# Kernel tuning notes

Measured on AMD Instinct MI355X. Metric: run time of the kernel, lower is better.

Reference implementation:

```python
import jax, jax.numpy as jnp
import numpy as np

NUM_EXPERTS = 8
TOP_K = 2

def setup_inputs() -> dict:
    key = jax.random.key(0)
    ks = jax.random.split(key, 5)
    B, S, D, F, E = 4, 2048, 1024, 4096, NUM_EXPERTS
    x = jax.random.normal(ks[0], (B, S, D), dtype=jnp.float32)
    router_w = jax.random.normal(ks[1], (D, E), dtype=jnp.float32) * 0.02
    router_b = jnp.zeros((E,), dtype=jnp.float32)
    w1 = jax.random.normal(ks[2], (E, D, F), dtype=jnp.float32) * 0.02
    b1 = jnp.zeros((E, F), dtype=jnp.float32)
    w2 = jax.random.normal(ks[3], (E, F, D), dtype=jnp.float32) * 0.02
    b2 = jnp.zeros((E, D), dtype=jnp.float32)
    return {"x": x, "router_w": router_w, "router_b": router_b,
            "w1": w1, "b1": b1, "w2": w2, "b2": b2}

def reference(x, router_w, router_b, w1, b1, w2, b2):
    B, S, D = x.shape
    E = router_w.shape[1]
    x_flat = x.reshape(-1, D)                                  # [N, D]
    router_probs = jax.nn.softmax(x_flat @ router_w + router_b, axis=-1)  # [N, E]
    topk_probs, topk_idx = jax.lax.top_k(router_probs, TOP_K)  # [N, K]
    topk_probs = topk_probs / jnp.sum(topk_probs, axis=-1, keepdims=True)
    # combine weight per (token, expert): sum over top-k slots assigned to that expert
    cw = jnp.sum(topk_probs[..., None] * jax.nn.one_hot(topk_idx, E, dtype=x.dtype), axis=1)  # [N, E]
    out = jnp.zeros_like(x_flat)
    for e in range(E):  # small fixed expert count; each iter is a dense GEMM pair
        h = jax.nn.gelu(x_flat @ w1[e] + b1[e], approximate=False)  # [N, F]
        out = out + cw[:, e:e + 1] * (h @ w2[e] + b2[e])            # [N, D]
    return out.reshape(B, S, D)
```

## Files before the change

kernel.cpp:

```cpp
#include <hip/hip_runtime.h>
#include <hip/hip_bf16.h>

typedef __attribute__((ext_vector_type(8))) __bf16 bf16x8;
typedef __attribute__((ext_vector_type(4))) float f32x4;

#define NTOK 8192
#define D_DIM 1024
#define F_DIM 4096
#define NEXP 8
#define SLOT_TOT 16384
#define SLOT_CAP 16640
#define TILE_MAX 136

__device__ __forceinline__ unsigned short f2b(float f) {
  __hip_bfloat16 b = __float2bfloat16(f);
  return reinterpret_cast<unsigned short&>(b);
}

__device__ __forceinline__ float gelu_f(float v) {
  const float y2 = v * (1.5957691216f + 0.0713548162f * v * v);
  return v * __builtin_amdgcn_rcpf(1.f + __expf(-y2));
}

__device__ __forceinline__ void gload_lds16(const void* g, void* l) {
  __builtin_amdgcn_global_load_lds(
      (__attribute__((address_space(1))) void*)g,
      (__attribute__((address_space(3))) void*)l, 16, 0, 0);
}


__global__ void init_counts_kernel(int* counts) {
  if (threadIdx.x < NEXP) counts[threadIdx.x] = 0;
}

__global__ void zero_out_kernel(float* out) {
  const int i = blockIdx.x * 256 + threadIdx.x;
  reinterpret_cast<float4*>(out)[i] = make_float4(0.f, 0.f, 0.f, 0.f);
}

__global__ void gather_x_kernel(const float* __restrict__ x,
                                const int* __restrict__ slot_token,
                                __hip_bfloat16* __restrict__ xg) {
  const int s = blockIdx.x;
  const int t = slot_token[s];
  const int d = threadIdx.x * 4;
  const float4 v = *reinterpret_cast<const float4*>(x + (size_t)t * D_DIM + d);
  union { unsigned short u[4]; uint2 q; } o;
  o.u[0] = f2b(v.x); o.u[1] = f2b(v.y); o.u[2] = f2b(v.z); o.u[3] = f2b(v.w);
  *reinterpret_cast<uint2*>(xg + (size_t)s * D_DIM + d) = o.q;
}

__global__ void combine_kernel(const __hip_bfloat16* __restrict__ ys,
                               const int* __restrict__ slot_pos,
                               const float* __restrict__ topk_w,
                               float* __restrict__ out) {
  const int tok = blockIdx.x;
  const int d = threadIdx.x * 4;
  const int s0 = slot_pos[tok * 2], s1 = slot_pos[tok * 2 + 1];
  const float w0 = topk_w[tok * 2], w1 = topk_w[tok * 2 + 1];
  union { unsigned short u[4]; uint2 q; } a, b;
  a.q = *reinterpret_cast<const uint2*>(ys + (size_t)s0 * D_DIM + d);
  b.q = *reinterpret_cast<const uint2*>(ys + (size_t)s1 * D_DIM + d);
  float4 rr;
  float va[4];
  #pragma unroll
  for (int i = 0; i < 4; ++i) {
    unsigned int ua = (unsigned int)a.u[i] << 16;
    unsigned int ub = (unsigned int)b.u[i] << 16;
    va[i] = w0 * reinterpret_cast<float&>(ua) + w1 * reinterpret_cast<float&>(ub);
  }
  rr.x = va[0]; rr.y = va[1]; rr.z = va[2]; rr.w = va[3];
  *reinterpret_cast<float4*>(out + (size_t)tok * D_DIM + d) = rr;
}

__global__ void transpose_conv_kernel(const float* __restrict__ src,
                                      __hip_bfloat16* __restrict__ dst,
                                      int R, int C) {
  __shared__ float tile[64][65];
  const int e = blockIdx.z;
  src += (size_t)e * R * C;
  dst += (size_t)e * R * C;
  const int c0 = blockIdx.x * 64, r0 = blockIdx.y * 64;
  const int tx = threadIdx.x, ty = threadIdx.y;
  #pragma unroll
  for (int j = 0; j < 4; ++j) {
    const float4 v = *reinterpret_cast<const float4*>(
        &src[(size_t)(r0 + ty + j * 16) * C + c0 + tx * 4]);
    tile[ty + j * 16][tx * 4 + 0] = v.x;
    tile[ty + j * 16][tx * 4 + 1] = v.y;
    tile[ty + j * 16][tx * 4 + 2] = v.z;
    tile[ty + j * 16][tx * 4 + 3] = v.w;
  }
  __syncthreads();
  #pragma unroll
  for (int j = 0; j < 4; ++j) {
    const int c = ty + j * 16;
    union { unsigned short u[4]; uint2 d; } o;
    #pragma unroll
    for (int i = 0; i < 4; ++i) o.u[i] = f2b(tile[tx * 4 + i][c]);
    *reinterpret_cast<uint2*>(&dst[(size_t)(c0 + c) * R + r0 + tx * 4]) = o.d;
  }
}

__global__ void router_kernel(const float* __restrict__ x,
                              const float* __restrict__ rw,
                              const float* __restrict__ rb,
                              int* __restrict__ topk_idx,
                              float* __restrict__ topk_w,
                              int* __restrict__ counts) {
  __shared__ float rwT[NEXP * D_DIM];
  const int tid = threadIdx.x;
  for (int i = tid; i < NEXP * D_DIM; i += 256) {
    const int d = i >> 3, e = i & 7;
    rwT[e * D_DIM + d] = rw[i];
  }
  __syncthreads();

  const int wave = tid >> 6, lane = tid & 63;
  const int tok = blockIdx.x * 4 + wave;
  const float* xr = x + (size_t)tok * D_DIM;

  float acc[NEXP];
  #pragma unroll
  for (int e = 0; e < NEXP; ++e) acc[e] = 0.f;

  for (int i = 0; i < D_DIM / 64; ++i) {
    const int d = i * 64 + lane;
    const float xv = xr[d];
    #pragma unroll
    for (int e = 0; e < NEXP; ++e) acc[e] += xv * rwT[e * D_DIM + d];
  }
  #pragma unroll
  for (int off = 32; off > 0; off >>= 1) {
    #pragma unroll
    for (int e = 0; e < NEXP; ++e) acc[e] += __shfl_xor(acc[e], off);
  }

  if (lane == 0) {
    float l[NEXP];
    #pragma unroll
    for (int e = 0; e < NEXP; ++e) l[e] = acc[e] + rb[e];
    int i1 = 0;
    #pragma unroll
    for (int e = 1; e < NEXP; ++e) if (l[e] > l[i1]) i1 = e;
    int i2 = (i1 == 0) ? 1 : 0;
    #pragma unroll
    for (int e = 0; e < NEXP; ++e) if (e != i1 && e != i2 && l[e] > l[i2]) i2 = e;
    const float w1 = 1.f / (1.f + __expf(l[i2] - l[i1]));
    topk_idx[tok * 2 + 0] = i1;
    topk_idx[tok * 2 + 1] = i2;
    topk_w[tok * 2 + 0] = w1;
    topk_w[tok * 2 + 1] = 1.f - w1;
    atomicAdd(&counts[i1], 1);
    atomicAdd(&counts[i2], 1);
  }
}

__global__ void offsets_kernel(const int* __restrict__ counts,
                               int* __restrict__ offsets,
                               int* __restrict__ cursors,
                               int* __restrict__ slot_token,
                               int* __restrict__ tile_meta) {
  const int t = threadIdx.x;
  if (t == 0) {
    int s = 0;
    for (int e = 0; e < NEXP; ++e) { offsets[e] = s; cursors[e] = s; s += counts[e]; }
    offsets[NEXP] = s;
    int n = 0;
    for (int e = 0; e < NEXP; ++e) {
      const int nt = (counts[e] + 127) >> 7;
      for (int m = 0; m < nt && n < TILE_MAX; ++m) tile_meta[n++] = e | (m << 8);
    }
    for (; n < TILE_MAX; ++n) tile_meta[n] = 0 | (1 << 22);
  }
  if (t < SLOT_CAP - SLOT_TOT) {
    slot_token[SLOT_TOT + t] = 0;
  }
}

__global__ void scatter_kernel(const int* __restrict__ topk_idx,
                               int* __restrict__ cursors,
                               int* __restrict__ slot_token,
                               int* __restrict__ slot_pos) {
  const int tok = blockIdx.x * 256 + threadIdx.x;
  if (tok >= NTOK) return;
  #pragma unroll
  for (int k = 0; k < 2; ++k) {
    const int e = topk_idx[tok * 2 + k];
    const int p = atomicAdd(&cursors[e], 1);
    slot_token[p] = tok;
    slot_pos[tok * 2 + k] = p;
  }
}

template <int PHASE>
__global__ __launch_bounds__(256, 5) void moe_gemm(
    const __hip_bfloat16* __restrict__ A,
    const __hip_bfloat16* __restrict__ B,
    const float* __restrict__ bias,
    const int* __restrict__ counts,
    const int* __restrict__ offsets,
    const int* __restrict__ tile_meta,
    __hip_bfloat16* __restrict__ Cout) {
  constexpr int K    = (PHASE == 1) ? D_DIM : F_DIM;
  constexpr int NCOL = (PHASE == 1) ? F_DIM : D_DIM;
  constexpr int NT   = NCOL / 128;
  constexpr int KT   = K / 32;

  const int bid = blockIdx.x;
  const int j = bid / NT, nt = bid % NT;
  const int meta = tile_meta[j];
  const int e = meta & 255, mt = meta >> 8;
  const int cnt = counts[e];
  if (mt * 128 >= cnt) return;
  const int base = offsets[e];

  __shared__ unsigned short lds[2][8192];

  const int tid = threadIdx.x;
  const int w = tid >> 6, lane = tid & 63;
  const int r = lane & 15, kg = lane >> 4;
  const int wm = w >> 1, wn = w & 1;

  const __hip_bfloat16* gA0 = A + (size_t)(base + mt * 128 + w * 16 + r) * K + kg * 8;
  const __hip_bfloat16* gA1 = gA0 + (size_t)64 * K;
  const __hip_bfloat16* gB0 = B + ((size_t)e * NCOL + nt * 128 + w * 16 + r) * K + kg * 8;
  const __hip_bfloat16* gB1 = gB0 + (size_t)64 * K;

  f32x4 acc[4][4] = {};

  auto stage = [&](unsigned short* buf) {
    gload_lds16(gA0, buf + w * 512);
    gload_lds16(gA1, buf + (w + 4) * 512);
    gload_lds16(gB0, buf + 4096 + w * 512);
    gload_lds16(gB1, buf + 4096 + (w + 4) * 512);
    gA0 += 32; gA1 += 32; gB0 += 32; gB1 += 32;
  };
  auto compute = [&](const unsigned short* buf) {
    bf16x8 af[4], bfr[4];
    #pragma unroll
    for (int i2 = 0; i2 < 4; ++i2) {
      af[i2]  = *(const bf16x8*)(buf + (wm * 4 + i2) * 512 + lane * 8);
      bfr[i2] = *(const bf16x8*)(buf + 4096 + (wn * 4 + i2) * 512 + lane * 8);
    }
    #pragma unroll
    for (int mi = 0; mi < 4; ++mi)
      #pragma unroll
      for (int ni = 0; ni < 4; ++ni)
        acc[mi][ni] = __builtin_amdgcn_mfma_f32_16x16x32_bf16(
            af[mi], bfr[ni], acc[mi][ni], 0, 0, 0);
  };

  unsigned short* pc = lds[0];
  unsigned short* pn = lds[1];

  stage(pc);
  for (int t = 0; t < KT - 1; ++t) {
    stage(pn);
    __builtin_amdgcn_sched_barrier(0);
    asm volatile("s_waitcnt vmcnt(4)" ::: "memory");
    __builtin_amdgcn_sched_barrier(0);
    __builtin_amdgcn_s_barrier();
    compute(pc);
    __builtin_amdgcn_sched_barrier(0);
    __builtin_amdgcn_s_barrier();
    unsigned short* ts = pc; pc = pn; pn = ts;
  }
  asm volatile("s_waitcnt vmcnt(0)" ::: "memory");
  __builtin_amdgcn_sched_barrier(0);
  __builtin_amdgcn_s_barrier();
  compute(pc);

  const int rem = cnt - mt * 128;
  const int q4 = (lane >> 4) * 4;
  const int c15 = lane & 15;

  if (rem >= 128) {
    #pragma unroll
    for (int n = 0; n < 4; ++n) {
      const int col = nt * 128 + wn * 64 + n * 16 + c15;
      const float bv = bias[e * NCOL + col];
      #pragma unroll
      for (int m = 0; m < 4; ++m) {
        #pragma unroll
        for (int rr = 0; rr < 4; ++rr) {
          const int rloc = wm * 64 + m * 16 + q4 + rr;
          float v = acc[m][n][rr] + bv;
          if constexpr (PHASE == 1) v = gelu_f(v);
          Cout[(size_t)(base + mt * 128 + rloc) * NCOL + col] = __float2bfloat16(v);
        }
      }
    }
  } else {
    #pragma unroll
    for (int n = 0; n < 4; ++n) {
      const int col = nt * 128 + wn * 64 + n * 16 + c15;
      const float bv = bias[e * NCOL + col];
      #pragma unroll
      for (int m = 0; m < 4; ++m) {
        #pragma unroll
        for (int rr = 0; rr < 4; ++rr) {
          const int rloc = wm * 64 + m * 16 + q4 + rr;
          if (rloc < rem) {
            float v = acc[m][n][rr] + bv;
            if constexpr (PHASE == 1) v = gelu_f(v);
            Cout[(size_t)(base + mt * 128 + rloc) * NCOL + col] = __float2bfloat16(v);
          }
        }
      }
    }
  }
}


extern "C" void kernel_launch(void* const* d_in, const int* in_sizes, int n_in,
                              void* d_out, int out_size, void* d_ws, size_t ws_size,
                              hipStream_t stream) {
  const float* x  = (const float*)d_in[0];
  const float* rw = (const float*)d_in[1];
  const float* rb = (const float*)d_in[2];
  const float* w1 = (const float*)d_in[3];
  const float* b1 = (const float*)d_in[4];
  const float* w2 = (const float*)d_in[5];
  const float* b2 = (const float*)d_in[6];
  float* out = (float*)d_out;

  char* p = (char*)d_ws;
  size_t used = 0;
  auto carve = [&](size_t bytes) {
    char* r = p + used;
    used += (bytes + 255) & ~(size_t)255;
    return (void*)r;
  };
  __hip_bfloat16* xg  = (__hip_bfloat16*)carve((size_t)SLOT_CAP * D_DIM * 2);
  __hip_bfloat16* ys  = xg;
  __hip_bfloat16* w1t = (__hip_bfloat16*)carve((size_t)NEXP * F_DIM * D_DIM * 2);
  __hip_bfloat16* w2t = (__hip_bfloat16*)carve((size_t)NEXP * D_DIM * F_DIM * 2);
  __hip_bfloat16* h   = (__hip_bfloat16*)carve((size_t)SLOT_CAP * F_DIM * 2);
  int*   topk_idx   = (int*)carve((size_t)NTOK * 2 * 4);
  float* topk_w     = (float*)carve((size_t)NTOK * 2 * 4);
  int*   slot_token = (int*)carve((size_t)SLOT_CAP * 4);
  int*   slot_pos   = (int*)carve((size_t)NTOK * 2 * 4);
  int*   tile_meta  = (int*)carve(TILE_MAX * 4);
  int* counts  = (int*)carve(256);
  int* offsets = (int*)carve(256);
  int* cursors = (int*)carve(256);

  if (used > ws_size) {
    zero_out_kernel<<<8192, 256, 0, stream>>>(out);
    return;
  }

  init_counts_kernel<<<1, 64, 0, stream>>>(counts);
  router_kernel<<<NTOK / 4, 256, 0, stream>>>(x, rw, rb, topk_idx, topk_w, counts);
  offsets_kernel<<<1, 256, 0, stream>>>(counts, offsets, cursors, slot_token, tile_meta);
  scatter_kernel<<<NTOK / 256, 256, 0, stream>>>(topk_idx, cursors, slot_token, slot_pos);
  gather_x_kernel<<<SLOT_CAP, 256, 0, stream>>>(x, slot_token, xg);

  dim3 tb(16, 16);
  transpose_conv_kernel<<<dim3(F_DIM / 64, D_DIM / 64, NEXP), tb, 0, stream>>>(w1, w1t, D_DIM, F_DIM);
  transpose_conv_kernel<<<dim3(D_DIM / 64, F_DIM / 64, NEXP), tb, 0, stream>>>(w2, w2t, F_DIM, D_DIM);

  moe_gemm<1><<<TILE_MAX * (F_DIM / 128), 256, 0, stream>>>(
      xg, w1t, b1, counts, offsets, tile_meta, h);
  moe_gemm<2><<<TILE_MAX * (D_DIM / 128), 256, 0, stream>>>(
      h, w2t, b2, counts, offsets, tile_meta, ys);

  combine_kernel<<<NTOK, 256, 0, stream>>>(ys, slot_pos, topk_w, out);
}
```

Measured before the change: 987.8 us.

## Fuse scatter into gather, relax GEMM occupancy and simplify pipeline barriers

Merges the scatter and gather kernels so each token block claims its two slots with atomics and writes its bf16 row to both, removing one launch and the slot_token indirection. The GEMM launch bound drops from 5 to 4 waves per SIMD, and the hand-tuned partial vmcnt waits plus two raw barriers become a single __syncthreads after compute. That barrier change likely forces a full wait on in-flight loads each iteration, which can lose the overlap between the next stage's loads and compute. Padding slots beyond SLOT_TOT are no longer initialised, so the gather leaves them untouched.

```diff
diff --git a/kernel.cpp b/kernel.cpp
--- a/kernel.cpp
+++ b/kernel.cpp
@@ -38,16 +38,27 @@
   reinterpret_cast<float4*>(out)[i] = make_float4(0.f, 0.f, 0.f, 0.f);
 }
 
-__global__ void gather_x_kernel(const float* __restrict__ x,
-                                const int* __restrict__ slot_token,
-                                __hip_bfloat16* __restrict__ xg) {
-  const int s = blockIdx.x;
-  const int t = slot_token[s];
-  const int d = threadIdx.x * 4;
-  const float4 v = *reinterpret_cast<const float4*>(x + (size_t)t * D_DIM + d);
+__global__ void scatter_gather_kernel(const float* __restrict__ x,
+                                      const int* __restrict__ topk_idx,
+                                      int* __restrict__ cursors,
+                                      int* __restrict__ slot_pos,
+                                      __hip_bfloat16* __restrict__ xg) {
+  __shared__ int ps[2];
+  const int tok = blockIdx.x;
+  const int tid = threadIdx.x;
+  if (tid < 2) {
+    const int e = topk_idx[tok * 2 + tid];
+    const int p = atomicAdd(&cursors[e], 1);
+    slot_pos[tok * 2 + tid] = p;
+    ps[tid] = p;
+  }
+  __syncthreads();
+  const int d = tid * 4;
+  const float4 v = *reinterpret_cast<const float4*>(x + (size_t)tok * D_DIM + d);
   union { unsigned short u[4]; uint2 q; } o;
   o.u[0] = f2b(v.x); o.u[1] = f2b(v.y); o.u[2] = f2b(v.z); o.u[3] = f2b(v.w);
-  *reinterpret_cast<uint2*>(xg + (size_t)s * D_DIM + d) = o.q;
+  *reinterpret_cast<uint2*>(xg + (size_t)ps[0] * D_DIM + d) = o.q;
+  *reinterpret_cast<uint2*>(xg + (size_t)ps[1] * D_DIM + d) = o.q;
 }
 
 __global__ void combine_kernel(const __hip_bfloat16* __restrict__ ys,
@@ -159,42 +170,22 @@
 __global__ void offsets_kernel(const int* __restrict__ counts,
                                int* __restrict__ offsets,
                                int* __restrict__ cursors,
-                               int* __restrict__ slot_token,
                                int* __restrict__ tile_meta) {
-  const int t = threadIdx.x;
-  if (t == 0) {
+  if (threadIdx.x == 0) {
     int s = 0;
     for (int e = 0; e < NEXP; ++e) { offsets[e] = s; cursors[e] = s; s += counts[e]; }
     offsets[NEXP] = s;
     int n = 0;
     for (int e = 0; e < NEXP; ++e) {
-      const int nt = (counts[e] + 127) >> 7;
-      for (int m = 0; m < nt && n < TILE_MAX; ++m) tile_meta[n++] = e | (m << 8);
+      const int ntile = (counts[e] + 127) >> 7;
+      for (int m = 0; m < ntile && n < TILE_MAX; ++m) tile_meta[n++] = e | (m << 8);
     }
     for (; n < TILE_MAX; ++n) tile_meta[n] = 0 | (1 << 22);
   }
-  if (t < SLOT_CAP - SLOT_TOT) {
-    slot_token[SLOT_TOT + t] = 0;
-  }
-}
-
-__global__ void scatter_kernel(const int* __restrict__ topk_idx,
-                               int* __restrict__ cursors,
-                               int* __restrict__ slot_token,
-                               int* __restrict__ slot_pos) {
-  const int tok = blockIdx.x * 256 + threadIdx.x;
-  if (tok >= NTOK) return;
-  #pragma unroll
-  for (int k = 0; k < 2; ++k) {
-    const int e = topk_idx[tok * 2 + k];
-    const int p = atomicAdd(&cursors[e], 1);
-    slot_token[p] = tok;
-    slot_pos[tok * 2 + k] = p;
-  }
 }
 
 template <int PHASE>
-__global__ __launch_bounds__(256, 5) void moe_gemm(
+__global__ __launch_bounds__(256, 4) void moe_gemm(
     const __hip_bfloat16* __restrict__ A,
     const __hip_bfloat16* __restrict__ B,
     const float* __restrict__ bias,
@@ -255,20 +246,13 @@
   unsigned short* pn = lds[1];
 
   stage(pc);
+  __syncthreads();
   for (int t = 0; t < KT - 1; ++t) {
     stage(pn);
-    __builtin_amdgcn_sched_barrier(0);
-    asm volatile("s_waitcnt vmcnt(4)" ::: "memory");
-    __builtin_amdgcn_sched_barrier(0);
-    __builtin_amdgcn_s_barrier();
     compute(pc);
-    __builtin_amdgcn_sched_barrier(0);
-    __builtin_amdgcn_s_barrier();
+    __syncthreads();
     unsigned short* ts = pc; pc = pn; pn = ts;
   }
-  asm volatile("s_waitcnt vmcnt(0)" ::: "memory");
-  __builtin_amdgcn_sched_barrier(0);
-  __builtin_amdgcn_s_barrier();
   compute(pc);
 
   const int rem = cnt - mt * 128;
@@ -339,7 +323,6 @@
   __hip_bfloat16* h   = (__hip_bfloat16*)carve((size_t)SLOT_CAP * F_DIM * 2);
   int*   topk_idx   = (int*)carve((size_t)NTOK * 2 * 4);
   float* topk_w     = (float*)carve((size_t)NTOK * 2 * 4);
-  int*   slot_token = (int*)carve((size_t)SLOT_CAP * 4);
   int*   slot_pos   = (int*)carve((size_t)NTOK * 2 * 4);
   int*   tile_meta  = (int*)carve(TILE_MAX * 4);
   int* counts  = (int*)carve(256);
@@ -353,9 +336,8 @@
 
   init_counts_kernel<<<1, 64, 0, stream>>>(counts);
   router_kernel<<<NTOK / 4, 256, 0, stream>>>(x, rw, rb, topk_idx, topk_w, counts);
-  offsets_kernel<<<1, 256, 0, stream>>>(counts, offsets, cursors, slot_token, tile_meta);
-  scatter_kernel<<<NTOK / 256, 256, 0, stream>>>(topk_idx, cursors, slot_token, slot_pos);
-  gather_x_kernel<<<SLOT_CAP, 256, 0, stream>>>(x, slot_token, xg);
+  offsets_kernel<<<1, 64, 0, stream>>>(counts, offsets, cursors, tile_meta);
+  scatter_gather_kernel<<<NTOK, 256, 0, stream>>>(x, topk_idx, cursors, slot_pos, xg);
 
   dim3 tb(16, 16);
   transpose_conv_kernel<<<dim3(F_DIM / 64, D_DIM / 64, NEXP), tb, 0, stream>>>(w1, w1t, D_DIM, F_DIM);
```

Measured after the change: 986.2 us. About the same (-0.2%).
